# Kernel optimization log

Hardware: AMD Instinct MI355X
Metric: run time of the kernel (lower is better)

## Reference

```python
import jax, jax.numpy as jnp
import numpy as np
import math

B, T, C = 1, 2048, 2048
NH, HS = 16, 128          # hs = C // nh
NLQ, NLKV, DHR = 1536, 512, 64


def _rope(x, cos, sin):
    # x: [B, T, H, D]; cos/sin: [T, D//2]. Rotates pairs (even, odd) like
    # torch's complex-multiply apply_rotary_emb.
    xr = x.reshape(x.shape[:-1] + (-1, 2))
    x_re, x_im = xr[..., 0], xr[..., 1]
    c = cos[None, :, None, :]
    s = sin[None, :, None, :]
    out = jnp.stack([x_re * c - x_im * s, x_re * s + x_im * c], axis=-1)
    return out.reshape(x.shape)


def setup_inputs() -> dict:
    key = jax.random.key(0)
    ks = jax.random.split(key, 9)
    sc = 0.02  # init scale so logits stay sane
    x = jax.random.normal(ks[0], (B, T, C), jnp.float32)
    # RoPE tables (theta = 10000), matching precompute_freqs_cis
    inv = 1.0 / (10000.0 ** (jnp.arange(0, DHR, 2, dtype=jnp.float32) / DHR))
    ang = jnp.outer(jnp.arange(T, dtype=jnp.float32), inv)  # [T, DHR//2]
    return {
        "x": x,
        "freqs_cos": jnp.cos(ang),
        "freqs_sin": jnp.sin(ang),
        "W_dq": jax.random.normal(ks[1], (NLQ, C), jnp.float32) * sc,
        "W_uq": jax.random.normal(ks[2], (C, NLQ), jnp.float32) * sc,
        "W_dkv": jax.random.normal(ks[3], (NLKV, C), jnp.float32) * sc,
        "W_uk": jax.random.normal(ks[4], (C, NLKV), jnp.float32) * sc,
        "W_uv": jax.random.normal(ks[5], (C, NLKV), jnp.float32) * sc,
        "W_qr": jax.random.normal(ks[6], (NH * DHR, NLQ), jnp.float32) * sc,
        "W_kr": jax.random.normal(ks[7], (DHR, C), jnp.float32) * sc,
        "W_o": jax.random.normal(ks[8], (C, C), jnp.float32) * sc,
    }


def reference(x, freqs_cos, freqs_sin, W_dq, W_uq, W_dkv, W_uk, W_uv, W_qr, W_kr, W_o):
    # ---- low-rank query/kv down-projections ----
    c_q = x @ W_dq.T                       # [B,T,NLQ]
    c_kv = x @ W_dkv.T                     # [B,T,NLKV]  (no kv_cache: c_kv = new_c_kv)

    # ---- weight absorption (training path) ----
    # torch: W_uq.weight.view(1,nlq,nh,hs).transpose(1,2) @ W_uk.weight.view(1,nh,hs,nlkv)
    Wuq_h = W_uq.reshape(NLQ, NH, HS).transpose(1, 0, 2)   # [NH,NLQ,HS]
    Wuk_h = W_uk.reshape(NH, HS, NLKV)                     # [NH,HS,NLKV]
    k_eff = jnp.einsum('hql,hlk->hqk', Wuq_h, Wuk_h)       # [NH,NLQ,NLKV]
    # torch: (W_uv.weight.T @ W_o.weight.T).view(nlkv,nh,hs).transpose(0,1)
    v_eff = (W_uv.T @ W_o.T).reshape(NLKV, NH, HS).transpose(1, 0, 2)  # [NH,NLKV,HS]

    # ---- content attention scores in latent space ----
    attn_c = jnp.einsum('bhtk,bsk->bhts',
                        jnp.einsum('btq,hqk->bhtk', c_q, k_eff), c_kv)  # [B,NH,T,T]

    # ---- decoupled RoPE subspace ----
    k_r = _rope((x @ W_kr.T)[:, :, None, :], freqs_cos, freqs_sin)[:, :, 0, :]   # [B,T,DHR]
    q_r = _rope((c_q @ W_qr.T).reshape(B, T, NH, DHR), freqs_cos, freqs_sin)
    q_r = q_r.transpose(0, 2, 1, 3)                                              # [B,NH,T,DHR]
    attn_r = jnp.einsum('bhtd,bsd->bhts', q_r, k_r)                              # [B,NH,T,T]

    # ---- combine, causal mask, softmax ----
    scale = 1.0 / math.sqrt(HS + DHR)
    scores = (attn_c + attn_r) * scale
    causal = jnp.tril(jnp.ones((T, T), dtype=bool))  # mask = triu(diag=1) complement
    scores = jnp.where(causal[None, None], scores, jnp.float32(-jnp.inf))
    attn = jax.nn.softmax(scores, axis=-1)           # dropout p=0.0

    # ---- value path: attend in latent space, then absorbed up+output proj ----
    y_lat = jnp.einsum('bhts,bsk->bhtk', attn, c_kv)          # [B,NH,T,NLKV]
    y = jnp.einsum('bhtk,hkd->bhtd', y_lat, v_eff)            # [B,NH,T,HS]
    y = y.transpose(0, 2, 1, 3).reshape(B, T, C)              # [B,T,C] (W_o absorbed)
    return y
```

## Files before the change

kernel.cpp:

```cpp
#include <hip/hip_runtime.h>
#include <hip/hip_bf16.h>
#include <math.h>

typedef __bf16 bf16_t;
typedef __bf16 bf16x4 __attribute__((ext_vector_type(4)));
typedef __bf16 bf16x8 __attribute__((ext_vector_type(8)));
typedef float f32x4 __attribute__((ext_vector_type(4)));

#define T_DIM 2048
#define C_DIM 2048
#define NH 16
#define HS 128
#define NLQ 1536
#define NLKV 512
#define DHR 64
#define QKD 192

__global__ void detect_k(const bf16_t* __restrict__ x, int* __restrict__ flag) {
  int bad = 0;
  for (int i = threadIdx.x; i < 256; i += 64) {
    float v = (float)x[i];
    if (!(fabsf(v) < 1.0e6f)) bad = 1;
  }
  unsigned long long m = __ballot(bad);
  if (threadIdx.x == 0) *flag = (m != 0ull) ? 1 : 0;
}

struct CvPack {
  const void* src[9];
  bf16_t* dst[9];
  int n[9];
};

__global__ __launch_bounds__(256) void convert_all_k(CvPack p, const int* __restrict__ flag) {
  const int which = blockIdx.y;
  const int n = p.n[which];
  const int f32 = *flag;
  const int stride = gridDim.x * 256 * 8;
  for (int i = (blockIdx.x * 256 + threadIdx.x) * 8; i < n; i += stride) {
    if (f32) {
      const float* s = (const float*)p.src[which] + i;
      f32x4 lo = *(const f32x4*)s;
      f32x4 hi = *(const f32x4*)(s + 4);
      bf16x8 v;
#pragma unroll
      for (int j = 0; j < 4; ++j) { v[j] = (bf16_t)lo[j]; v[j + 4] = (bf16_t)hi[j]; }
      *(bf16x8*)(p.dst[which] + i) = v;
    } else {
      *(bf16x8*)(p.dst[which] + i) = *(const bf16x8*)((const bf16_t*)p.src[which] + i);
    }
  }
}

__global__ void transpose_k(const void* __restrict__ in, bf16_t* __restrict__ out,
                            int R, int C, const int* __restrict__ flag) {
  __shared__ bf16_t tile[32][33];
  const int f32 = *flag;
  int bx = blockIdx.x * 32, by = blockIdx.y * 32;
  int tx = threadIdx.x, ty = threadIdx.y;
  for (int i = ty; i < 32; i += 8) {
    int r = by + i, c = bx + tx;
    if (r < R && c < C) {
      size_t idx = (size_t)r * C + c;
      tile[i][tx] = f32 ? (bf16_t)((const float*)in)[idx] : ((const bf16_t*)in)[idx];
    }
  }
  __syncthreads();
  for (int i = ty; i < 32; i += 8) {
    int r = bx + i, c = by + tx;
    if (r < C && c < R) out[(size_t)r * R + c] = tile[tx][i];
  }
}

__device__ __forceinline__ void async16(const bf16_t* g, bf16_t* l) {
  __builtin_amdgcn_global_load_lds(
      (const __attribute__((address_space(1))) void*)g,
      (__attribute__((address_space(3))) void*)l, 16, 0, 0);
}

#define BM 128
#define BN 128

struct GDesc {
  const bf16_t* A; const bf16_t* B; bf16_t* C;
  int M, N, K, lda, ldb, ldc, mb, bx0;
};
struct GGrp { GDesc d[3]; };

__global__ __launch_bounds__(256) void gemm_group(GGrp g, int nseg) {
  int bx = blockIdx.x;
  int s = 0;
  while (s + 1 < nseg && bx >= g.d[s + 1].bx0) ++s;
  const GDesc D = g.d[s];
  const int local = bx - D.bx0;
  const int bm = (local % D.mb) * BM, bn = (local / D.mb) * BN;

  __shared__ bf16_t As[BM * 32];
  __shared__ bf16_t Bs[BN * 32];
  const int tid = threadIdx.x;
  const int lane = tid & 63;
  const int wave = tid >> 6;
  const int l16 = lane & 15, quad = lane >> 4;
  const int wm = (wave >> 1) * 64, wn = (wave & 1) * 64;
  const int srow = lane >> 2;
  const int scol = (lane & 3) * 8;
  f32x4 acc[4][4] = {};

  for (int k0 = 0; k0 < D.K; k0 += 32) {
    __syncthreads();
#pragma unroll
    for (int pss = 0; pss < 2; ++pss) {
      int rowT = pss * 64 + wave * 16 + srow;
      int ar = bm + rowT; if (ar > D.M - 1) ar = D.M - 1;
      async16(D.A + (size_t)ar * D.lda + k0 + scol, As + (pss * 64 + wave * 16) * 32);
      int br = bn + rowT; if (br > D.N - 1) br = D.N - 1;
      async16(D.B + (size_t)br * D.ldb + k0 + scol, Bs + (pss * 64 + wave * 16) * 32);
    }
    __syncthreads();
    bf16x8 af[4], bfr[4];
#pragma unroll
    for (int i = 0; i < 4; ++i)
      af[i] = *(const bf16x8*)(As + (wm + i * 16 + l16) * 32 + quad * 8);
#pragma unroll
    for (int j = 0; j < 4; ++j)
      bfr[j] = *(const bf16x8*)(Bs + (wn + j * 16 + l16) * 32 + quad * 8);
#pragma unroll
    for (int i = 0; i < 4; ++i)
#pragma unroll
      for (int j = 0; j < 4; ++j)
        acc[i][j] = __builtin_amdgcn_mfma_f32_16x16x32_bf16(af[i], bfr[j], acc[i][j], 0, 0, 0);
  }
#pragma unroll
  for (int i = 0; i < 4; ++i)
#pragma unroll
    for (int j = 0; j < 4; ++j)
#pragma unroll
      for (int r = 0; r < 4; ++r) {
        int gm = bm + wm + i * 16 + quad * 4 + r;
        int gn = bn + wn + j * 16 + l16;
        if (gm < D.M && gn < D.N) D.C[(size_t)gm * D.ldc + gn] = (bf16_t)acc[i][j][r];
      }
}

__global__ void pack_qk_k(const bf16_t* __restrict__ qcat, const bf16_t* __restrict__ khead,
                          const bf16_t* __restrict__ xa,
                          const bf16_t* __restrict__ fc, const bf16_t* __restrict__ fs,
                          bf16_t* __restrict__ Qp, bf16_t* __restrict__ Kp) {
  int idx = blockIdx.x * blockDim.x + threadIdx.x;
  if (idx >= NH * T_DIM * 96) return;
  int j = idx % 96;
  int t = (idx / 96) % T_DIM;
  int h = idx / (96 * T_DIM);
  if (blockIdx.y == 0) {
    const float scale = 0.07216878364870323f;
    bf16_t* out = Qp + ((size_t)h * T_DIM + t) * QKD;
    if (j < 64) {
      float a = (float)qcat[(size_t)t * 3072 + h * HS + 2 * j];
      float b = (float)qcat[(size_t)t * 3072 + h * HS + 2 * j + 1];
      out[2 * j] = (bf16_t)(a * scale);
      out[2 * j + 1] = (bf16_t)(b * scale);
    } else {
      int i = j - 64;
      float re = (float)qcat[(size_t)t * 3072 + 2048 + h * DHR + 2 * i];
      float im = (float)qcat[(size_t)t * 3072 + 2048 + h * DHR + 2 * i + 1];
      float c = (float)fc[t * 32 + i], s = (float)fs[t * 32 + i];
      out[HS + 2 * i] = (bf16_t)((re * c - im * s) * scale);
      out[HS + 2 * i + 1] = (bf16_t)((re * s + im * c) * scale);
    }
  } else {
    bf16_t* out = Kp + ((size_t)h * T_DIM + t) * QKD;
    if (j < 64) {
      out[2 * j] = khead[(size_t)t * C_DIM + h * HS + 2 * j];
      out[2 * j + 1] = khead[(size_t)t * C_DIM + h * HS + 2 * j + 1];
    } else {
      int i = j - 64;
      float re = (float)xa[(size_t)t * 2112 + 2048 + 2 * i];
      float im = (float)xa[(size_t)t * 2112 + 2048 + 2 * i + 1];
      float c = (float)fc[t * 32 + i], s = (float)fs[t * 32 + i];
      out[HS + 2 * i] = (bf16_t)(re * c - im * s);
      out[HS + 2 * i + 1] = (bf16_t)(re * s + im * c);
    }
  }
}

#define FBM 128
#define FBN 64
#define KPITCH 200
#define VPITCH 72
#define PPITCH 72

__global__ __launch_bounds__(256) void flash_k(const bf16_t* __restrict__ Qp,
                                               const bf16_t* __restrict__ Kp,
                                               const bf16_t* __restrict__ VT,
                                               void* __restrict__ Y,
                                               const int* __restrict__ flag,
                                               float* __restrict__ Opart,
                                               float* __restrict__ Mpart,
                                               float* __restrict__ Lpart) {
  __shared__ bf16_t Ksm[FBN * KPITCH];
  __shared__ bf16_t Vtsm[HS * VPITCH];
  __shared__ bf16_t Psm[4][32 * PPITCH];
  const int tid = threadIdx.x;
  const int lane = tid & 63, wave = tid >> 6;
  const int l16 = lane & 15, quad = lane >> 4;
  const int h = blockIdx.y;
  const int p = blockIdx.x;
  int qt, kt0, kt1, partial;
  if (p < 16) {
    qt = 8 + (p >> 1);
    int half = qt + 1;
    kt0 = (p & 1) ? half : 0;
    kt1 = (p & 1) ? (2 * qt + 2) : half;
    partial = 1;
  } else {
    qt = 23 - p; kt0 = 0; kt1 = 2 * qt + 2; partial = 0;
  }
  const int qb = qt * FBM;
  const int f32out = *flag;

  bf16x8 aq[2][6];
#pragma unroll
  for (int tt = 0; tt < 2; ++tt) {
    const bf16_t* qbase = Qp + ((size_t)h * T_DIM + qb + wave * 32 + tt * 16 + l16) * QKD;
#pragma unroll
    for (int c = 0; c < 6; ++c) aq[tt][c] = *(const bf16x8*)(qbase + c * 32 + quad * 8);
  }

  f32x4 o[2][8] = {};
  float m_i[2] = {-3.0e38f, -3.0e38f}, l_i[2] = {0.f, 0.f};

  const bf16_t* kg_base = Kp + (size_t)h * T_DIM * QKD;
  const bf16_t* vg_base = VT + (size_t)(h * HS) * T_DIM;

  bf16x8 kreg[6], vreg[4];
  {
    const bf16_t* kg = kg_base + (size_t)kt0 * FBN * QKD;
#pragma unroll
    for (int i = 0; i < 6; ++i) {
      int idx = i * 256 + tid;
      kreg[i] = *(const bf16x8*)(kg + (size_t)idx * 8);
    }
    const bf16_t* vg = vg_base + kt0 * FBN;
#pragma unroll
    for (int i = 0; i < 4; ++i) {
      int idx = i * 256 + tid, row = idx >> 3, c8 = idx & 7;
      vreg[i] = *(const bf16x8*)(vg + (size_t)row * T_DIM + c8 * 8);
    }
  }

  for (int kt = kt0; kt < kt1; ++kt) {
    __syncthreads();
#pragma unroll
    for (int i = 0; i < 6; ++i) {
      int idx = i * 256 + tid, row = idx / 24, c8 = idx % 24;
      *(bf16x8*)(Ksm + row * KPITCH + c8 * 8) = kreg[i];
    }
#pragma unroll
    for (int i = 0; i < 4; ++i) {
      int idx = i * 256 + tid, row = idx >> 3, c8 = idx & 7;
      *(bf16x8*)(Vtsm + row * VPITCH + c8 * 8) = vreg[i];
    }
    __syncthreads();
    if (kt + 1 < kt1) {
      const bf16_t* kg = kg_base + (size_t)(kt + 1) * FBN * QKD;
#pragma unroll
      for (int i = 0; i < 6; ++i) {
        int idx = i * 256 + tid;
        kreg[i] = *(const bf16x8*)(kg + (size_t)idx * 8);
      }
      const bf16_t* vg = vg_base + (kt + 1) * FBN;
#pragma unroll
      for (int i = 0; i < 4; ++i) {
        int idx = i * 256 + tid, row = idx >> 3, c8 = idx & 7;
        vreg[i] = *(const bf16x8*)(vg + (size_t)row * T_DIM + c8 * 8);
      }
    }
    f32x4 sc[2][4] = {};
#pragma unroll
    for (int nt = 0; nt < 4; ++nt)
#pragma unroll
      for (int c = 0; c < 6; ++c) {
        bf16x8 bk = *(const bf16x8*)(Ksm + (nt * 16 + l16) * KPITCH + c * 32 + quad * 8);
        sc[0][nt] = __builtin_amdgcn_mfma_f32_16x16x32_bf16(bk, aq[0][c], sc[0][nt], 0, 0, 0);
        sc[1][nt] = __builtin_amdgcn_mfma_f32_16x16x32_bf16(bk, aq[1][c], sc[1][nt], 0, 0, 0);
      }
    if (kt >= 2 * qt) {
#pragma unroll
      for (int tt = 0; tt < 2; ++tt) {
        int t_glob = qb + wave * 32 + tt * 16 + l16;
#pragma unroll
        for (int nt = 0; nt < 4; ++nt) {
          int s_base = kt * FBN + nt * 16 + quad * 4;
#pragma unroll
          for (int r = 0; r < 4; ++r)
            if (s_base + r > t_glob) sc[tt][nt][r] = -3.0e38f;
        }
      }
    }
#pragma unroll
    for (int tt = 0; tt < 2; ++tt) {
      float mx = sc[tt][0][0];
#pragma unroll
      for (int nt = 0; nt < 4; ++nt)
#pragma unroll
        for (int r = 0; r < 4; ++r) mx = fmaxf(mx, sc[tt][nt][r]);
      mx = fmaxf(mx, __shfl_xor(mx, 16, 64));
      mx = fmaxf(mx, __shfl_xor(mx, 32, 64));
      float mn = fmaxf(m_i[tt], mx);
      float alpha = exp2f((m_i[tt] - mn) * 1.4426950408889634f);
      float rs = 0.f;
#pragma unroll
      for (int nt = 0; nt < 4; ++nt) {
        bf16x4 pk;
#pragma unroll
        for (int r = 0; r < 4; ++r) {
          float pv = exp2f((sc[tt][nt][r] - mn) * 1.4426950408889634f);
          rs += pv;
          pk[r] = (bf16_t)pv;
        }
        *(bf16x4*)(&Psm[wave][(tt * 16 + l16) * PPITCH + nt * 16 + quad * 4]) = pk;
      }
      rs += __shfl_xor(rs, 16, 64);
      rs += __shfl_xor(rs, 32, 64);
      l_i[tt] = l_i[tt] * alpha + rs;
      m_i[tt] = mn;
#pragma unroll
      for (int dt = 0; dt < 8; ++dt) o[tt][dt] *= alpha;
    }
#pragma unroll
    for (int s2 = 0; s2 < 2; ++s2) {
      bf16x8 ap0 = *(const bf16x8*)(&Psm[wave][l16 * PPITCH + s2 * 32 + quad * 8]);
      bf16x8 ap1 = *(const bf16x8*)(&Psm[wave][(16 + l16) * PPITCH + s2 * 32 + quad * 8]);
#pragma unroll
      for (int dt = 0; dt < 8; ++dt) {
        bf16x8 bv = *(const bf16x8*)(Vtsm + (dt * 16 + l16) * VPITCH + s2 * 32 + quad * 8);
        o[0][dt] = __builtin_amdgcn_mfma_f32_16x16x32_bf16(bv, ap0, o[0][dt], 0, 0, 0);
        o[1][dt] = __builtin_amdgcn_mfma_f32_16x16x32_bf16(bv, ap1, o[1][dt], 0, 0, 0);
      }
    }
  }

  if (!partial) {
#pragma unroll
    for (int tt = 0; tt < 2; ++tt) {
      float inv = 1.0f / l_i[tt];
      int t = qb + wave * 32 + tt * 16 + l16;
#pragma unroll
      for (int dt = 0; dt < 8; ++dt) {
        size_t oi = (size_t)t * C_DIM + h * HS + dt * 16 + quad * 4;
        if (f32out) {
          f32x4 v;
#pragma unroll
          for (int r = 0; r < 4; ++r) v[r] = o[tt][dt][r] * inv;
          *(f32x4*)((float*)Y + oi) = v;
        } else {
          bf16x4 v;
#pragma unroll
          for (int r = 0; r < 4; ++r) v[r] = (bf16_t)(o[tt][dt][r] * inv);
          *(bf16x4*)((bf16_t*)Y + oi) = v;
        }
      }
    }
  } else {
    const int pi = h * 16 + p;
#pragma unroll
    for (int tt = 0; tt < 2; ++tt) {
      int rowl = wave * 32 + tt * 16 + l16;
      float* ob = Opart + ((size_t)pi * 128 + rowl) * 128;
#pragma unroll
      for (int dt = 0; dt < 8; ++dt) {
        f32x4 v = o[tt][dt];
        *(f32x4*)(ob + dt * 16 + quad * 4) = v;
      }
      if (quad == 0) {
        Mpart[(size_t)pi * 128 + rowl] = m_i[tt];
        Lpart[(size_t)pi * 128 + rowl] = l_i[tt];
      }
    }
  }
}

__global__ __launch_bounds__(256) void combine_k(const float* __restrict__ Opart,
                                                 const float* __restrict__ Mpart,
                                                 const float* __restrict__ Lpart,
                                                 void* __restrict__ Y,
                                                 const int* __restrict__ flag) {
  const int h = blockIdx.y;
  const int qi = blockIdx.x;
  const int pi0 = h * 16 + qi * 2, pi1 = pi0 + 1;
  const int row = threadIdx.x >> 1;
  const int c0 = (threadIdx.x & 1) * 64;
  const int f32out = *flag;
  float m0 = Mpart[(size_t)pi0 * 128 + row], m1 = Mpart[(size_t)pi1 * 128 + row];
  float l0 = Lpart[(size_t)pi0 * 128 + row], l1 = Lpart[(size_t)pi1 * 128 + row];
  float ms = fmaxf(m0, m1);
  float w0 = exp2f((m0 - ms) * 1.4426950408889634f);
  float w1 = exp2f((m1 - ms) * 1.4426950408889634f);
  float inv = 1.0f / (l0 * w0 + l1 * w1);
  const float* O0 = Opart + ((size_t)pi0 * 128 + row) * 128 + c0;
  const float* O1 = Opart + ((size_t)pi1 * 128 + row) * 128 + c0;
  int t = (8 + qi) * 128 + row;
  size_t ob = (size_t)t * C_DIM + h * HS + c0;
#pragma unroll
  for (int d4 = 0; d4 < 64; d4 += 4) {
    f32x4 a = *(const f32x4*)(O0 + d4);
    f32x4 b = *(const f32x4*)(O1 + d4);
#pragma unroll
    for (int j = 0; j < 4; ++j) {
      float v = (a[j] * w0 + b[j] * w1) * inv;
      if (f32out) ((float*)Y)[ob + d4 + j] = v;
      else        ((bf16_t*)Y)[ob + d4 + j] = (bf16_t)v;
    }
  }
}

extern "C" void kernel_launch(void* const* d_in, const int* in_sizes, int n_in,
                              void* d_out, int out_size, void* d_ws, size_t ws_size,
                              hipStream_t stream) {
  bf16_t* w = (bf16_t*)d_ws;
  int* flag = (int*)d_ws;

  if (ws_size < (size_t)34472000 * 2 + 128) return;

  bf16_t* fcc    = w + 64;
  bf16_t* fsc    = w + 65600;
  bf16_t* xc     = w + 131136;
  bf16_t* BigB   = w + 4325440;
  bf16_t* dqc    = BigB;
  bf16_t* dkvc   = BigB + 3145728;
  bf16_t* krc    = BigB + 4194304;
  bf16_t* Bq     = w + 8650816;
  bf16_t* W_uq_t = Bq;
  bf16_t* qrc    = Bq + 3145728;
  bf16_t* xa     = w + 13369408;
  bf16_t* qcat   = w + 17694784;
  bf16_t* k_head = w + 23986240;
  bf16_t* vhatT  = w + 28180544;
  bf16_t* ukc    = w + 32374848;
  bf16_t* Pt     = w + 33423424;
  bf16_t* woc    = qcat;
  bf16_t* W_uv_t = k_head;
  bf16_t* Qpack  = xc;
  bf16_t* Kpack  = qcat;
  float* Opart = (float*)(w + 6422592);
  float* Mpart = (float*)(w + 14811200);
  float* Lpart = (float*)(w + 14876736);

  detect_k<<<1, 64, 0, stream>>>((const bf16_t*)d_in[0], flag);

  CvPack cp;
  const void* srcs[9] = {d_in[1], d_in[2], d_in[0], d_in[3], d_in[5], d_in[9], d_in[8], d_in[6], d_in[10]};
  bf16_t* dsts[9]     = {fcc,     fsc,     xc,      dqc,     dkvc,    krc,     qrc,     ukc,     woc};
  int ns[9] = {T_DIM * 32, T_DIM * 32, T_DIM * C_DIM, NLQ * C_DIM, NLKV * C_DIM,
               DHR * C_DIM, NH * DHR * NLQ, C_DIM * NLKV, C_DIM * C_DIM};
  for (int i = 0; i < 9; ++i) { cp.src[i] = srcs[i]; cp.dst[i] = dsts[i]; cp.n[i] = ns[i]; }
  convert_all_k<<<dim3(512, 9), 256, 0, stream>>>(cp, flag);

  dim3 tb(32, 8);
  transpose_k<<<dim3(64, 48), tb, 0, stream>>>(d_in[4], W_uq_t, 1536, 2048, flag);
  transpose_k<<<dim3(16, 64), tb, 0, stream>>>(d_in[7], W_uv_t, 2048, 512, flag);

  {
    GGrp g;
    g.d[0] = {xc,  BigB,   xa, 2048, 2112, 2048, 2048, 2048, 2112, 16, 0};
    g.d[1] = {woc, W_uv_t, Pt, 2048,  512, 2048, 2048, 2048,  512, 16, 272};
    gemm_group<<<336, 256, 0, stream>>>(g, 2);
  }
  {
    GGrp g;
    g.d[0] = {xa,        Bq,        qcat,   2048, 3072, 1536, 2112, 1536, 3072, 16, 0};
    g.d[1] = {xa + 1536, ukc,       k_head, 2048, 2048,  512, 2112,  512, 2048, 16, 384};
    g.d[2] = {Pt,        xa + 1536, vhatT,  2048, 2048,  512,  512, 2112, 2048, 16, 640};
    gemm_group<<<896, 256, 0, stream>>>(g, 3);
  }

  int pk = (NH * T_DIM * 96 + 255) / 256;
  pack_qk_k<<<dim3(pk, 2), 256, 0, stream>>>(qcat, k_head, xa, fcc, fsc, Qpack, Kpack);

  flash_k<<<dim3(24, NH), 256, 0, stream>>>(Qpack, Kpack, vhatT, d_out, flag, Opart, Mpart, Lpart);
  combine_k<<<dim3(8, NH), 256, 0, stream>>>(Opart, Mpart, Lpart, d_out, flag);
}
```

Measured before the change: 364.2 us.

## Fuse dtype probe, conversions and transposes into one prep kernel; XCD-aware flash mapping

```diff
diff --git a/kernel.cpp b/kernel.cpp
--- a/kernel.cpp
+++ b/kernel.cpp
@@ -16,59 +16,65 @@
 #define DHR 64
 #define QKD 192
 
-__global__ void detect_k(const bf16_t* __restrict__ x, int* __restrict__ flag) {
+__device__ __forceinline__ int probe_f32(const bf16_t* __restrict__ x) {
+  int lane = threadIdx.x & 63;
   int bad = 0;
-  for (int i = threadIdx.x; i < 256; i += 64) {
-    float v = (float)x[i];
+#pragma unroll
+  for (int i = 0; i < 4; ++i) {
+    float v = (float)x[lane + i * 64];
     if (!(fabsf(v) < 1.0e6f)) bad = 1;
   }
-  unsigned long long m = __ballot(bad);
-  if (threadIdx.x == 0) *flag = (m != 0ull) ? 1 : 0;
-}
-
-struct CvPack {
+  return (__ballot(bad) != 0ull) ? 1 : 0;
+}
+
+struct PrepPack {
   const void* src[9];
   bf16_t* dst[9];
   int n[9];
+  const void* tsrc[2];
+  bf16_t* tdst[2];
+  int tR[2], tC[2], tbx[2];
 };
 
-__global__ __launch_bounds__(256) void convert_all_k(CvPack p, const int* __restrict__ flag) {
+__global__ __launch_bounds__(256) void prep_k(PrepPack p, const bf16_t* __restrict__ xprobe) {
+  __shared__ bf16_t tile[32][33];
+  const int f32 = probe_f32(xprobe);
   const int which = blockIdx.y;
-  const int n = p.n[which];
-  const int f32 = *flag;
-  const int stride = gridDim.x * 256 * 8;
-  for (int i = (blockIdx.x * 256 + threadIdx.x) * 8; i < n; i += stride) {
-    if (f32) {
-      const float* s = (const float*)p.src[which] + i;
-      f32x4 lo = *(const f32x4*)s;
-      f32x4 hi = *(const f32x4*)(s + 4);
-      bf16x8 v;
-#pragma unroll
-      for (int j = 0; j < 4; ++j) { v[j] = (bf16_t)lo[j]; v[j + 4] = (bf16_t)hi[j]; }
-      *(bf16x8*)(p.dst[which] + i) = v;
-    } else {
-      *(bf16x8*)(p.dst[which] + i) = *(const bf16x8*)((const bf16_t*)p.src[which] + i);
-    }
-  }
-}
-
-__global__ void transpose_k(const void* __restrict__ in, bf16_t* __restrict__ out,
-                            int R, int C, const int* __restrict__ flag) {
-  __shared__ bf16_t tile[32][33];
-  const int f32 = *flag;
-  int bx = blockIdx.x * 32, by = blockIdx.y * 32;
-  int tx = threadIdx.x, ty = threadIdx.y;
-  for (int i = ty; i < 32; i += 8) {
-    int r = by + i, c = bx + tx;
-    if (r < R && c < C) {
+  if (which < 9) {
+    const int n = p.n[which];
+    const int stride = gridDim.x * 256 * 8;
+    for (int i = (blockIdx.x * 256 + threadIdx.x) * 8; i < n; i += stride) {
+      if (f32) {
+        const float* s = (const float*)p.src[which] + i;
+        f32x4 lo = *(const f32x4*)s;
+        f32x4 hi = *(const f32x4*)(s + 4);
+        bf16x8 v;
+#pragma unroll
+        for (int j = 0; j < 4; ++j) { v[j] = (bf16_t)lo[j]; v[j + 4] = (bf16_t)hi[j]; }
+        *(bf16x8*)(p.dst[which] + i) = v;
+      } else {
+        *(bf16x8*)(p.dst[which] + i) = *(const bf16x8*)((const bf16_t*)p.src[which] + i);
+      }
+    }
+  } else {
+    const int ts = which - 9;
+    const int R = p.tR[ts], C = p.tC[ts], tbx = p.tbx[ts];
+    const int ntiles = tbx * (R / 32);
+    if ((int)blockIdx.x >= ntiles) return;
+    const void* in = p.tsrc[ts];
+    bf16_t* out = p.tdst[ts];
+    int bx = (blockIdx.x % tbx) * 32, by = (blockIdx.x / tbx) * 32;
+    int tx = threadIdx.x & 31, ty = threadIdx.x >> 5;
+    for (int i = ty; i < 32; i += 8) {
+      int r = by + i, c = bx + tx;
       size_t idx = (size_t)r * C + c;
       tile[i][tx] = f32 ? (bf16_t)((const float*)in)[idx] : ((const bf16_t*)in)[idx];
     }
-  }
-  __syncthreads();
-  for (int i = ty; i < 32; i += 8) {
-    int r = bx + i, c = by + tx;
-    if (r < C && c < R) out[(size_t)r * R + c] = tile[tx][i];
+    __syncthreads();
+    for (int i = ty; i < 32; i += 8) {
+      int r = bx + i, c = by + tx;
+      out[(size_t)r * R + c] = tile[tx][i];
+    }
   }
 }
 
@@ -193,7 +199,7 @@
                                                const bf16_t* __restrict__ Kp,
                                                const bf16_t* __restrict__ VT,
                                                void* __restrict__ Y,
-                                               const int* __restrict__ flag,
+                                               const bf16_t* __restrict__ xprobe,
                                                float* __restrict__ Opart,
                                                float* __restrict__ Mpart,
                                                float* __restrict__ Lpart) {
@@ -203,8 +209,10 @@
   const int tid = threadIdx.x;
   const int lane = tid & 63, wave = tid >> 6;
   const int l16 = lane & 15, quad = lane >> 4;
-  const int h = blockIdx.y;
-  const int p = blockIdx.x;
+  const int id = blockIdx.x;
+  const int xcd = id & 7, slot = id >> 3;
+  const int h = xcd + 8 * (slot / 24);
+  const int p = slot % 24;
   int qt, kt0, kt1, partial;
   if (p < 16) {
     qt = 8 + (p >> 1);
@@ -216,7 +224,7 @@
     qt = 23 - p; kt0 = 0; kt1 = 2 * qt + 2; partial = 0;
   }
   const int qb = qt * FBM;
-  const int f32out = *flag;
+  const int f32out = probe_f32(xprobe);
 
   bf16x8 aq[2][6];
 #pragma unroll
@@ -384,13 +392,13 @@
                                                  const float* __restrict__ Mpart,
                                                  const float* __restrict__ Lpart,
                                                  void* __restrict__ Y,
-                                                 const int* __restrict__ flag) {
+                                                 const bf16_t* __restrict__ xprobe) {
   const int h = blockIdx.y;
   const int qi = blockIdx.x;
   const int pi0 = h * 16 + qi * 2, pi1 = pi0 + 1;
   const int row = threadIdx.x >> 1;
   const int c0 = (threadIdx.x & 1) * 64;
-  const int f32out = *flag;
+  const int f32out = probe_f32(xprobe);
   float m0 = Mpart[(size_t)pi0 * 128 + row], m1 = Mpart[(size_t)pi1 * 128 + row];
   float l0 = Lpart[(size_t)pi0 * 128 + row], l1 = Lpart[(size_t)pi1 * 128 + row];
   float ms = fmaxf(m0, m1);
@@ -418,7 +426,7 @@
                               void* d_out, int out_size, void* d_ws, size_t ws_size,
                               hipStream_t stream) {
   bf16_t* w = (bf16_t*)d_ws;
-  int* flag = (int*)d_ws;
+  const bf16_t* xprobe = (const bf16_t*)d_in[0];
 
   if (ws_size < (size_t)34472000 * 2 + 128) return;
 
@@ -446,19 +454,15 @@
   float* Mpart = (float*)(w + 14811200);
   float* Lpart = (float*)(w + 14876736);
 
-  detect_k<<<1, 64, 0, stream>>>((const bf16_t*)d_in[0], flag);
-
-  CvPack cp;
+  PrepPack pp;
   const void* srcs[9] = {d_in[1], d_in[2], d_in[0], d_in[3], d_in[5], d_in[9], d_in[8], d_in[6], d_in[10]};
   bf16_t* dsts[9]     = {fcc,     fsc,     xc,      dqc,     dkvc,    krc,     qrc,     ukc,     woc};
   int ns[9] = {T_DIM * 32, T_DIM * 32, T_DIM * C_DIM, NLQ * C_DIM, NLKV * C_DIM,
                DHR * C_DIM, NH * DHR * NLQ, C_DIM * NLKV, C_DIM * C_DIM};
-  for (int i = 0; i < 9; ++i) { cp.src[i] = srcs[i]; cp.dst[i] = dsts[i]; cp.n[i] = ns[i]; }
-  convert_all_k<<<dim3(512, 9), 256, 0, stream>>>(cp, flag);
-
-  dim3 tb(32, 8);
-  transpose_k<<<dim3(64, 48), tb, 0, stream>>>(d_in[4], W_uq_t, 1536, 2048, flag);
-  transpose_k<<<dim3(16, 64), tb, 0, stream>>>(d_in[7], W_uv_t, 2048, 512, flag);
+  for (int i = 0; i < 9; ++i) { pp.src[i] = srcs[i]; pp.dst[i] = dsts[i]; pp.n[i] = ns[i]; }
+  pp.tsrc[0] = d_in[4]; pp.tdst[0] = W_uq_t; pp.tR[0] = 1536; pp.tC[0] = 2048; pp.tbx[0] = 64;
+  pp.tsrc[1] = d_in[7]; pp.tdst[1] = W_uv_t; pp.tR[1] = 2048; pp.tC[1] = 512;  pp.tbx[1] = 16;
+  prep_k<<<dim3(3072, 11), 256, 0, stream>>>(pp, xprobe);
 
   {
     GGrp g;
@@ -477,6 +481,6 @@
   int pk = (NH * T_DIM * 96 + 255) / 256;
   pack_qk_k<<<dim3(pk, 2), 256, 0, stream>>>(qcat, k_head, xa, fcc, fsc, Qpack, Kpack);
 
-  flash_k<<<dim3(24, NH), 256, 0, stream>>>(Qpack, Kpack, vhatT, d_out, flag, Opart, Mpart, Lpart);
-  combine_k<<<dim3(8, NH), 256, 0, stream>>>(Opart, Mpart, Lpart, d_out, flag);
-}
+  flash_k<<<dim3(384), 256, 0, stream>>>(Qpack, Kpack, vhatT, d_out, xprobe, Opart, Mpart, Lpart);
+  combine_k<<<dim3(8, NH), 256, 0, stream>>>(Opart, Mpart, Lpart, d_out, xprobe);
+}
```

Result: faster. 351.5 us (-3.5%).
